# Kernel tuning notes

Measured on AMD Instinct MI355X. Metric: run time of the kernel, lower is better.

The kernel has to match this reference:

```python
import jax, jax.numpy as jnp
import numpy as np

N_LABELS = 2048
N_CLASSES = 2
BATCH = 2048
BRANCH = 4


def _tree():
    # deterministic rooted tree: parent(i) = (i-1)//BRANCH, node 0 is root
    parent = np.full(N_LABELS, -1, dtype=np.int64)
    parent[1:] = (np.arange(1, N_LABELS) - 1) // BRANCH
    depth = np.zeros(N_LABELS, dtype=np.int64)
    for i in range(1, N_LABELS):
        depth[i] = depth[parent[i]] + 1
    levels = [np.where(depth == d)[0] for d in range(int(depth.max()) + 1)]
    return parent, levels

_PARENT, _LEVELS = _tree()  # static structure (from the adjacency init arg)


def setup_inputs() -> dict:
    key = jax.random.key(0)
    k1, k2 = jax.random.split(key)
    emissions = jax.random.normal(k1, (BATCH, N_CLASSES, N_LABELS), dtype=jnp.float32)
    pairs = jax.random.normal(k2, (N_LABELS, N_LABELS, N_CLASSES, N_CLASSES), dtype=jnp.float32)
    return {"emissions": emissions, "pairs": pairs}


def _messages(emissions, pairs, upward):
    """Belief-propagation messages, level-synchronous (topological order).

    upward=True  -> alphas: messages from children to parents (leaves->root)
    upward=False -> betas:  messages from parents to children (root->leaves)
    """
    B, C, L = emissions.shape
    acc = jnp.zeros((B, C, L), emissions.dtype)
    if upward:
        # process deepest level first; all nodes at level d send to their
        # (level d-1) parents; duplicate parent indices accumulate via .add
        for d in range(len(_LEVELS) - 1, 0, -1):
            nodes = _LEVELS[d]      # senders (children), (K,)
            par = _PARENT[nodes]    # receivers (parents), (K,)
            # local[b, k, yc] = emissions[b, yc, node_k] + acc[b, yc, node_k]
            local = (emissions[:, :, nodes] + acc[:, :, nodes]).transpose(0, 2, 1)
            trans = pairs[par, nodes]  # (K, Cp, Cc): pairs[parent, child]
            # msg[b, k, yp] = logsumexp_yc( trans[k, yp, yc] + local[b, k, yc] )
            msg = jax.nn.logsumexp(trans[None] + local[:, :, None, :], axis=-1)
            acc = acc.at[:, :, par].add(msg.transpose(0, 2, 1))
    else:
        # process shallow -> deep; each node receives from its parent,
        # whose betas were completed in the previous level iteration
        for d in range(1, len(_LEVELS)):
            nodes = _LEVELS[d]      # receivers (children)
            par = _PARENT[nodes]    # senders (parents)
            local = (emissions[:, :, par] + acc[:, :, par]).transpose(0, 2, 1)  # (B,K,Cp)
            trans = pairs[nodes, par]  # (K, Cc, Cp): pairs[child, parent]
            msg = jax.nn.logsumexp(trans[None] + local[:, :, None, :], axis=-1)  # (B,K,Cc)
            acc = acc.at[:, :, nodes].add(msg.transpose(0, 2, 1))
    return acc


def reference(emissions, pairs):
    alphas = _messages(emissions, pairs, True)
    betas = _messages(emissions, pairs, False)
    scores = emissions + alphas + betas  # (B, C, L)
    # normalize over classes per label -> log marginals log p(y_i | X)
    return scores - jax.nn.logsumexp(scores, axis=1, keepdims=True)
```

## Files before the change

### kernel.cpp

```cpp
#include <hip/hip_runtime.h>


constexpr int NLAB = 2048;
constexpr int NBATCH = 2048;

#define LOG2E 1.4426950408889634f
#define LN2   0.6931471805599453f

__device__ __forceinline__ float fexp2(float x) { return __builtin_amdgcn_exp2f(x); }
__device__ __forceinline__ float flog2(float x) { return __builtin_amdgcn_logf(x); }

__global__ __launch_bounds__(256) void compact_pairs(
    const float4* __restrict__ pairs4,
    float4* __restrict__ up,
    float4* __restrict__ down)
{
    int i = blockIdx.x * 256 + threadIdx.x;
    if (i < NLAB - 1) {
        int c = i + 1, p = i >> 2;
        float4 t = pairs4[(size_t)p * NLAB + c];
        up[i] = make_float4(t.x, t.z,
                            fexp2((t.y - t.x) * LOG2E),
                            fexp2((t.w - t.z) * LOG2E));
        float4 s = pairs4[(size_t)c * NLAB + p];
        down[i] = make_float4(s.x, s.z,
                              fexp2((s.y - s.x) * LOG2E),
                              fexp2((s.w - s.z) * LOG2E));
    }
}

__global__ __launch_bounds__(64) void treecrf_kernel(
    const float* __restrict__ em_g,
    const float4* __restrict__ up,
    const float4* __restrict__ down,
    float* __restrict__ out)
{
    __shared__ float al[2 * 512];
    float2* al2 = reinterpret_cast<float2*>(al);

    const int b = blockIdx.x;
    const int lane = threadIdx.x;
    const float* __restrict__ e0g = em_g + (size_t)b * 2 * NLAB;
    const float* __restrict__ e1g = e0g + NLAB;

    const int ustart[6] = {1364, 340, 84, 20, 4, 0};
    const int uend[6]   = {2048, 1364, 340, 84, 20, 4};
#pragma unroll
    for (int pass = 0; pass < 6; ++pass) {
        for (int i = ustart[pass] + lane; i < uend[pass]; i += 64) {
            const bool valid = (i + 1) < NLAB;
            const int c = valid ? i + 1 : NLAB - 1;
            float l0 = e0g[c];
            float l1 = e1g[c];
            if (pass > 0) {
                float2 a = al2[min(c, 511)];
                bool internal = c < 512;
                l0 += internal ? a.x : 0.f;
                l1 += internal ? a.y : 0.f;
            }
            float4 t = up[min(i, NLAB - 2)];
            float eu = fexp2((l1 - l0) * LOG2E);
            float m0 = t.x + l0 + LN2 * flog2(fmaf(eu, t.z, 1.f));
            float m1 = t.y + l0 + LN2 * flog2(fmaf(eu, t.w, 1.f));
            if (!valid) { m0 = 0.f; m1 = 0.f; }
            m0 += __shfl_xor(m0, 1, 4);  m0 += __shfl_xor(m0, 2, 4);
            m1 += __shfl_xor(m1, 1, 4);  m1 += __shfl_xor(m1, 2, 4);
            if ((i & 3) == 0)
                al2[i >> 2] = make_float2(m0, m1);
        }
    }

    float* __restrict__ ob0 = out + (size_t)b * 2 * NLAB;
    float* __restrict__ ob1 = ob0 + NLAB;

    if (lane == 0) {
        float pb0 = e0g[0];
        float pb1 = e1g[0];
        float s0 = pb0 + al[0];
        float s1 = pb1 + al[1];
        float Z = s0 + LN2 * flog2(1.f + fexp2((s1 - s0) * LOG2E));
        ob0[0] = s0 - Z;
        ob1[0] = s1 - Z;
        al2[0] = make_float2(pb0, pb1);
    }

    const int dstart[6] = {1, 5, 21, 85, 341, 1365};
    const int dend[6]   = {5, 21, 85, 341, 1365, 2048};
#pragma unroll
    for (int pass = 0; pass < 6; ++pass) {
        for (int n = dstart[pass] + lane; n < dend[pass]; n += 64) {
            const int par = (n - 1) >> 2;
            float2 pp = al2[par];
            float4 t = down[n - 1];
            float eu = fexp2((pp.y - pp.x) * LOG2E);
            float m0 = t.x + pp.x + LN2 * flog2(fmaf(eu, t.z, 1.f));
            float m1 = t.y + pp.x + LN2 * flog2(fmaf(eu, t.w, 1.f));
            float a0 = 0.f, a1 = 0.f;
            if (pass < 5) {
                float2 a = al2[min(n, 511)];
                if (n < 512) { a0 = a.x; a1 = a.y; }
            }
            float pb0 = e0g[n] + m0;
            float pb1 = e1g[n] + m1;
            if (pass < 5 && n < 512)
                al2[n] = make_float2(pb0, pb1);
            float s0 = pb0 + a0;
            float s1 = pb1 + a1;
            float Z = s0 + LN2 * flog2(1.f + fexp2((s1 - s0) * LOG2E));
            ob0[n] = s0 - Z;
            ob1[n] = s1 - Z;
        }
    }
}

extern "C" void kernel_launch(void* const* d_in, const int* in_sizes, int n_in,
                              void* d_out, int out_size, void* d_ws, size_t ws_size,
                              hipStream_t stream) {
    const float*  emissions = (const float*)d_in[0];
    const float4* pairs4    = (const float4*)d_in[1];
    float* outp             = (float*)d_out;

    float4* upw = (float4*)d_ws;
    float4* dnw = upw + (NLAB - 1);
    compact_pairs<<<dim3((NLAB + 255) / 256), dim3(256), 0, stream>>>(pairs4, upw, dnw);
    treecrf_kernel<<<dim3(NBATCH), dim3(64), 0, stream>>>(emissions, upw, dnw, outp);
}
```

Baseline: 149.8 us.

## Stage per-batch emissions in shared memory and fully unroll level loops

Each block now loads its batch row of emissions into LDS with coalesced float4 loads, interleaved as (class0,class1) pairs. Later reads become single float2 LDS accesses instead of scattered global loads on the dependent chain. The per-level loops are fully unrolled with compile-time trip counts and active masks, and per-pass bounds checks are specialised. Launch bounds now request two blocks per CU. The cost is 16KB more LDS per block, which may limit occupancy, plus larger code from unrolling.

```diff
diff --git a/kernel.cpp b/kernel.cpp
--- a/kernel.cpp
+++ b/kernel.cpp
@@ -29,34 +29,52 @@
     }
 }
 
-__global__ __launch_bounds__(64) void treecrf_kernel(
+__global__ __launch_bounds__(64, 2) void treecrf_kernel(
     const float* __restrict__ em_g,
     const float4* __restrict__ up,
     const float4* __restrict__ down,
     float* __restrict__ out)
 {
+    __shared__ float em[2 * NLAB];
     __shared__ float al[2 * 512];
-    float2* al2 = reinterpret_cast<float2*>(al);
 
     const int b = blockIdx.x;
     const int lane = threadIdx.x;
-    const float* __restrict__ e0g = em_g + (size_t)b * 2 * NLAB;
-    const float* __restrict__ e1g = e0g + NLAB;
+    const float4* __restrict__ eg4 =
+        reinterpret_cast<const float4*>(em_g + (size_t)b * 2 * NLAB);
+    float4* em4 = reinterpret_cast<float4*>(em);
+    const float2* em2 = reinterpret_cast<const float2*>(em);
+    float2* al2 = reinterpret_cast<float2*>(al);
+
+#pragma unroll
+    for (int k = 0; k < 8; ++k) {
+        int j = k * 64 + lane;
+        float4 a0 = eg4[j];
+        float4 a1 = eg4[512 + j];
+        em4[2 * j]     = make_float4(a0.x, a1.x, a0.y, a1.y);
+        em4[2 * j + 1] = make_float4(a0.z, a1.z, a0.w, a1.w);
+    }
 
     const int ustart[6] = {1364, 340, 84, 20, 4, 0};
-    const int uend[6]   = {2048, 1364, 340, 84, 20, 4};
+    const int ucnt[6]   = {684, 1024, 256, 64, 16, 4};
 #pragma unroll
     for (int pass = 0; pass < 6; ++pass) {
-        for (int i = ustart[pass] + lane; i < uend[pass]; i += 64) {
-            const bool valid = (i + 1) < NLAB;
-            const int c = valid ? i + 1 : NLAB - 1;
-            float l0 = e0g[c];
-            float l1 = e1g[c];
-            if (pass > 0) {
+        const int s = ustart[pass];
+        const int iters = (ucnt[pass] + 63) >> 6;
+#pragma unroll
+        for (int k = 0; k < iters; ++k) {
+            const int i = s + k * 64 + lane;
+            const bool active = (i - s) < ucnt[pass];
+            const bool valid = active && (i + 1) < NLAB;
+            const int c = min(i + 1, NLAB - 1);
+            float2 e = em2[c];
+            float l0 = e.x, l1 = e.y;
+            if (pass == 1) {
                 float2 a = al2[min(c, 511)];
-                bool internal = c < 512;
-                l0 += internal ? a.x : 0.f;
-                l1 += internal ? a.y : 0.f;
+                if (c < 512) { l0 += a.x; l1 += a.y; }
+            } else if (pass >= 2) {
+                float2 a = al2[c];
+                l0 += a.x; l1 += a.y;
             }
             float4 t = up[min(i, NLAB - 2)];
             float eu = fexp2((l1 - l0) * LOG2E);
@@ -65,7 +83,7 @@
             if (!valid) { m0 = 0.f; m1 = 0.f; }
             m0 += __shfl_xor(m0, 1, 4);  m0 += __shfl_xor(m0, 2, 4);
             m1 += __shfl_xor(m1, 1, 4);  m1 += __shfl_xor(m1, 2, 4);
-            if ((i & 3) == 0)
+            if (active && (i & 3) == 0)
                 al2[i >> 2] = make_float2(m0, m1);
         }
     }
@@ -74,41 +92,54 @@
     float* __restrict__ ob1 = ob0 + NLAB;
 
     if (lane == 0) {
-        float pb0 = e0g[0];
-        float pb1 = e1g[0];
-        float s0 = pb0 + al[0];
-        float s1 = pb1 + al[1];
+        float2 e = em2[0];
+        float s0 = e.x + al[0];
+        float s1 = e.y + al[1];
         float Z = s0 + LN2 * flog2(1.f + fexp2((s1 - s0) * LOG2E));
         ob0[0] = s0 - Z;
         ob1[0] = s1 - Z;
-        al2[0] = make_float2(pb0, pb1);
+        al2[0] = make_float2(e.x, e.y);
     }
 
     const int dstart[6] = {1, 5, 21, 85, 341, 1365};
-    const int dend[6]   = {5, 21, 85, 341, 1365, 2048};
+    const int dcnt[6]   = {4, 16, 64, 256, 1024, 683};
 #pragma unroll
     for (int pass = 0; pass < 6; ++pass) {
-        for (int n = dstart[pass] + lane; n < dend[pass]; n += 64) {
-            const int par = (n - 1) >> 2;
+        const int s = dstart[pass];
+        const int iters = (dcnt[pass] + 63) >> 6;
+#pragma unroll
+        for (int k = 0; k < iters; ++k) {
+            const int n = s + k * 64 + lane;
+            const bool active = (n - s) < dcnt[pass];
+            const int nc = active ? n : s;
+            const int par = (nc - 1) >> 2;
             float2 pp = al2[par];
-            float4 t = down[n - 1];
+            float4 t = down[nc - 1];
             float eu = fexp2((pp.y - pp.x) * LOG2E);
             float m0 = t.x + pp.x + LN2 * flog2(fmaf(eu, t.z, 1.f));
             float m1 = t.y + pp.x + LN2 * flog2(fmaf(eu, t.w, 1.f));
+            float2 e = em2[nc];
+            float pb0 = e.x + m0;
+            float pb1 = e.y + m1;
             float a0 = 0.f, a1 = 0.f;
-            if (pass < 5) {
-                float2 a = al2[min(n, 511)];
-                if (n < 512) { a0 = a.x; a1 = a.y; }
+            if (pass <= 3) {
+                float2 a = al2[nc];
+                a0 = a.x; a1 = a.y;
+                if (active) al2[nc] = make_float2(pb0, pb1);
+            } else if (pass == 4) {
+                float2 a = al2[min(nc, 511)];
+                if (nc < 512) {
+                    a0 = a.x; a1 = a.y;
+                    if (active) al2[nc] = make_float2(pb0, pb1);
+                }
             }
-            float pb0 = e0g[n] + m0;
-            float pb1 = e1g[n] + m1;
-            if (pass < 5 && n < 512)
-                al2[n] = make_float2(pb0, pb1);
             float s0 = pb0 + a0;
             float s1 = pb1 + a1;
             float Z = s0 + LN2 * flog2(1.f + fexp2((s1 - s0) * LOG2E));
-            ob0[n] = s0 - Z;
-            ob1[n] = s1 - Z;
+            if (active) {
+                ob0[n] = s0 - Z;
+                ob1[n] = s1 - Z;
+            }
         }
     }
 }
```

New measurement: 138.1 us. 7.8% less time.
